# Performance work log

Hardware: AMD Instinct MI355X
Metric: run time of the kernel (lower is better)

Reference implementation:

```python
import jax, jax.numpy as jnp
import numpy as np

LOG2 = 0.6931471805599453
GAMMA = 10.0
NUM_KERNELS = 301
N_LAYERS = 3


def ssp(v):
    # ShiftedSoftplus: softplus(x) - log(2)
    return jax.nn.softplus(v) - jnp.asarray(LOG2, v.dtype)


def setup_inputs() -> dict:
    key = jax.random.key(0)
    ks = jax.random.split(key, 20)
    N, F, K, L, V = 512, 128, NUM_KERNELS, N_LAYERS, 100
    s = 0.05
    return {
        "x": jax.random.randint(ks[0], (N,), 0, V),
        "r": jax.random.uniform(ks[1], (N, 3), dtype=jnp.float32) * 10.0,
        "emb": jax.random.normal(ks[2], (V, F), dtype=jnp.float32),
        "aw_W": jax.random.normal(ks[3], (L, F, F), dtype=jnp.float32) * s,
        "aw_b": jax.random.normal(ks[4], (L, F), dtype=jnp.float32) * s,
        "cf_W1": jax.random.normal(ks[5], (L, K, F), dtype=jnp.float32) * s,
        "cf_b1": jax.random.normal(ks[6], (L, F), dtype=jnp.float32) * s,
        "cf_W2": jax.random.normal(ks[7], (L, F, F), dtype=jnp.float32) * s,
        "cf_b2": jax.random.normal(ks[8], (L, F), dtype=jnp.float32) * s,
        "n_W1": jax.random.normal(ks[9], (L, F, F), dtype=jnp.float32) * s,
        "n_b1": jax.random.normal(ks[10], (L, F), dtype=jnp.float32) * s,
        "n_W2": jax.random.normal(ks[11], (L, F, F), dtype=jnp.float32) * s,
        "n_b2": jax.random.normal(ks[12], (L, F), dtype=jnp.float32) * s,
        "out_W1": jax.random.normal(ks[13], (F, 32), dtype=jnp.float32) * s,
        "out_b1": jax.random.normal(ks[14], (32,), dtype=jnp.float32) * s,
        "out_W2": jax.random.normal(ks[15], (32, 1), dtype=jnp.float32) * s,
        "out_b2": jax.random.normal(ks[16], (1,), dtype=jnp.float32) * s,
    }


def reference(x, r, emb, aw_W, aw_b, cf_W1, cf_b1, cf_W2, cf_b2,
              n_W1, n_b1, n_W2, n_b2, out_W1, out_b1, out_W2, out_b2):
    centers = jnp.linspace(0.0, 30.0, NUM_KERNELS, dtype=r.dtype)  # [K]
    # pairwise distances (torch.cdist, p=2) with safe sqrt at the diagonal
    diff = r[:, None, :] - r[None, :, :]                 # [N,N,3]
    d2 = jnp.sum(diff * diff, axis=-1)                   # [N,N]
    mask = d2 > 0
    d = jnp.where(mask, jnp.sqrt(jnp.where(mask, d2, 1.0)), 0.0)

    h = emb[x]                                           # [N,F]
    for l in range(N_LAYERS):
        o = h @ aw_W[l] + aw_b[l]                        # atom-wise linear
        # Gaussian RBF expansion: [N,N,K]
        e = jnp.exp(-GAMMA * jnp.square(d[..., None] - centers))
        # filter-generating MLP: [N,N,F]
        w = ssp(e @ cf_W1[l] + cf_b1[l])
        w = ssp(w @ cf_W2[l] + cf_b2[l])
        # continuous-filter conv: o[i,k] = sum_j x[j,k] * w[i,j,k]
        c = jnp.einsum('jk,ijk->ik', o, w)
        c = ssp(c @ n_W1[l] + n_b1[l]) @ n_W2[l] + n_b2[l]
        h = h + c
    out = ssp(h @ out_W1 + out_b1) @ out_W2 + out_b2     # [N,1]
    # AdaptiveAvgPool1d(1) on a 2D [N,1] tensor is identity over L=1
    return out.reshape(-1)
```

## Files before the change

### kernel.cpp

```cpp
#include <hip/hip_runtime.h>
#include <hip/hip_fp16.h>
#include <math.h>

#define N_ATOMS 512
#define F_DIM   128
#define K_RBF   301
#define NLAYER  3
#define GAMMA_C 10.0f
#define LOG2_C  0.6931471805599453f

#define TAB_H     0.01f
#define TAB_INVH  100.0f
#define TAB_ROWS  1768
#define RPB       8
#define NGROUPS   (TAB_ROWS / RPB)
#define NTASKS    (NGROUPS * NLAYER)
#define NBBLK     ((NTASKS + 1) / 2)
#define ROW_BYTES 512

__device__ __forceinline__ float ssp(float x) {
    float ax = fabsf(x);
    return fmaxf(x, 0.0f) + log1pf(expf(-ax)) - LOG2_C;
}
__device__ __forceinline__ __half2 u2h2(unsigned u) {
    union { unsigned u; __half2 h; } c; c.u = u; return c.h;
}
__device__ __forceinline__ unsigned h22u(__half2 h) {
    union { unsigned u; __half2 h; } c; c.h = h; return c.u;
}

__global__ void __launch_bounds__(256)
prep_build(const int* __restrict__ x, const float* __restrict__ r,
           const float* __restrict__ emb,
           const float* __restrict__ aw_W, const float* __restrict__ aw_b,
           const float* __restrict__ cf_W1, const float* __restrict__ cf_b1,
           const float* __restrict__ cf_W2, const float* __restrict__ cf_b2,
           uint2* __restrict__ dpk, float* __restrict__ h,
           unsigned* __restrict__ opk, uint2* __restrict__ ptab) {
    __shared__ float hs[F_DIM];
    __shared__ float os[F_DIM];
    __shared__ float e_s[2][RPB + 1][34];
    __shared__ float w1_s[2][F_DIM][12];
    __shared__ float outs[2][RPB + 1][F_DIM];

    if (blockIdx.x < N_ATOMS) {
        int i = blockIdx.x;
        int t = threadIdx.x;
        float rx = r[i * 3 + 0], ry = r[i * 3 + 1], rz = r[i * 3 + 2];
        if (t < F_DIM) {
            float hv = emb[x[i] * F_DIM + t];
            h[i * F_DIM + t] = hv;
            hs[t] = hv;
        }
        for (int j = t; j < N_ATOMS; j += 256) {
            float dx = rx - r[j * 3 + 0];
            float dy = ry - r[j * 3 + 1];
            float dz = rz - r[j * 3 + 2];
            float d  = sqrtf(dx * dx + dy * dy + dz * dz);
            float xb = d * TAB_INVH;
            int   b  = ::min((int)xb, TAB_ROWS - 2);
            float fr = xb - (float)b;
            __half fh = __float2half(fr);
            dpk[i * N_ATOMS + j] = make_uint2((unsigned)b * ROW_BYTES,
                                              h22u(__halves2half2(fh, fh)));
        }
        __syncthreads();
        if (t < F_DIM) {
            float acc = aw_b[t];
            for (int g = 0; g < F_DIM; ++g) acc = fmaf(hs[g], aw_W[g * F_DIM + t], acc);
            os[t] = acc;
        }
        __syncthreads();
        if (t < F_DIM / 2)
            opk[i * 64 + t] = h22u(__halves2half2(__float2half(os[2 * t]),
                                                  __float2half(os[2 * t + 1])));
        return;
    }

    int u = threadIdx.x >> 7;
    int f = threadIdx.x & 127;
    int task = (blockIdx.x - N_ATOMS) * 2 + u;
    bool valid = task < NTASKS;
    task = ::min(task, NTASKS - 1);
    int l    = task / NGROUPS;
    int row0 = (task % NGROUPS) * RPB;

    float dlo = row0 * TAB_H;
    float dhi = (row0 + RPB) * TAB_H;
    int k0 = ::max(0, (int)ceilf((dlo - 1.45f) * 10.0f));
    int k1 = ::min(K_RBF - 1, (int)floorf((dhi + 1.45f) * 10.0f));
    int kw = k1 - k0 + 1;

    for (int idx = f; idx < (RPB + 1) * kw; idx += F_DIM) {
        int rr = idx / kw, kk = idx % kw;
        float dv = (row0 + rr) * TAB_H;
        float tt = dv - 0.1f * (float)(k0 + kk);
        e_s[u][rr][kk] = expf(-GAMMA_C * tt * tt);
    }
    __syncthreads();

    const float* W1 = cf_W1 + l * K_RBF * F_DIM;
    float b1v = cf_b1[l * F_DIM + f];
    float acc[RPB + 1];
#pragma unroll
    for (int rr = 0; rr <= RPB; ++rr) acc[rr] = b1v;
    for (int kk = 0; kk < kw; ++kk) {
        float w1v = W1[(k0 + kk) * F_DIM + f];
#pragma unroll
        for (int rr = 0; rr <= RPB; ++rr) acc[rr] = fmaf(e_s[u][rr][kk], w1v, acc[rr]);
    }
#pragma unroll
    for (int rr = 0; rr <= RPB; ++rr) w1_s[u][f][rr] = ssp(acc[rr]);
    __syncthreads();

    const float* W2 = cf_W2 + l * F_DIM * F_DIM;
    float b2v = cf_b2[l * F_DIM + f];
    float acc2[RPB + 1];
#pragma unroll
    for (int rr = 0; rr <= RPB; ++rr) acc2[rr] = b2v;
    for (int g = 0; g < F_DIM; ++g) {
        float w2v = W2[g * F_DIM + f];
        float4 wa = *(const float4*)&w1_s[u][g][0];
        float4 wb = *(const float4*)&w1_s[u][g][4];
        float  wc = w1_s[u][g][8];
        acc2[0] = fmaf(wa.x, w2v, acc2[0]);
        acc2[1] = fmaf(wa.y, w2v, acc2[1]);
        acc2[2] = fmaf(wa.z, w2v, acc2[2]);
        acc2[3] = fmaf(wa.w, w2v, acc2[3]);
        acc2[4] = fmaf(wb.x, w2v, acc2[4]);
        acc2[5] = fmaf(wb.y, w2v, acc2[5]);
        acc2[6] = fmaf(wb.z, w2v, acc2[6]);
        acc2[7] = fmaf(wb.w, w2v, acc2[7]);
        acc2[8] = fmaf(wc,   w2v, acc2[8]);
    }
#pragma unroll
    for (int rr = 0; rr <= RPB; ++rr) outs[u][rr][f] = ssp(acc2[rr]);
    __syncthreads();

    if (valid) {
        int p = f & 63;
        int rbase = (f >> 6) * (RPB / 2);
#pragma unroll
        for (int q = 0; q < RPB / 2; ++q) {
            int rr = rbase + q;
            float t00 = outs[u][rr][2 * p],     t01 = outs[u][rr][2 * p + 1];
            float n00 = outs[u][rr + 1][2 * p], n01 = outs[u][rr + 1][2 * p + 1];
            uint2 v = make_uint2(
                h22u(__halves2half2(__float2half(t00), __float2half(t01))),
                h22u(__halves2half2(__float2half(n00 - t00), __float2half(n01 - t01))));
            ptab[((size_t)l * TAB_ROWS + row0 + rr) * 64 + p] = v;
        }
    }
}

__global__ void __launch_bounds__(512)
convnode_kernel(const uint2* __restrict__ dpk, const unsigned* __restrict__ opk_in,
                const uint2* __restrict__ ptab,
                const float* __restrict__ n_W1, const float* __restrict__ n_b1,
                const float* __restrict__ n_W2, const float* __restrict__ n_b2,
                float* __restrict__ h,
                const float* __restrict__ aw_W, const float* __restrict__ aw_b,
                unsigned* __restrict__ opk_out,
                const float* __restrict__ oW1, const float* __restrict__ ob1,
                const float* __restrict__ oW2, const float* __restrict__ ob2,
                float* __restrict__ out, int l) {
    int i  = blockIdx.x;
    int t  = threadIdx.x;
    int p  = t & 63;
    int jc = t >> 6;

    __shared__ uint2  ds[N_ATOMS];
    __shared__ float2 red[8][64];
    __shared__ float  cs[F_DIM];
    __shared__ float  t1s[F_DIM];
    __shared__ float  hs[F_DIM];

    ds[t] = dpk[i * N_ATOMS + t];
    if (t < F_DIM) hs[t] = h[i * F_DIM + t];
    __syncthreads();

    const char* T = (const char*)(ptab + (size_t)l * TAB_ROWS * 64) + p * 8;
    float2 acc = make_float2(0.0f, 0.0f);
    int j = jc * 64;
#pragma unroll 4
    for (int jj = 0; jj < 64; ++jj, ++j) {
        uint2 e = ds[j];
        uint2 tv = *(const uint2*)(T + e.x);
        __half2 w2 = __hfma2(u2h2(e.y), u2h2(tv.y), u2h2(tv.x));
        __half2 oh = u2h2(opk_in[j * 64 + p]);
        acc.x = fmaf(__half2float(__low2half(w2)),  __half2float(__low2half(oh)),  acc.x);
        acc.y = fmaf(__half2float(__high2half(w2)), __half2float(__high2half(oh)), acc.y);
    }
    red[jc][p] = acc;
    __syncthreads();
    if (jc == 0) {
        float2 s = red[0][p];
#pragma unroll
        for (int q = 1; q < 8; ++q) { s.x += red[q][p].x; s.y += red[q][p].y; }
        *(float2*)&cs[2 * p] = s;
    }
    __syncthreads();

    if (t < F_DIM) {
        const float* W1 = n_W1 + l * F_DIM * F_DIM;
        float a = n_b1[l * F_DIM + t];
        for (int g = 0; g < F_DIM; ++g) a = fmaf(cs[g], W1[g * F_DIM + t], a);
        t1s[t] = ssp(a);
    }
    __syncthreads();
    if (t < F_DIM) {
        const float* W2 = n_W2 + l * F_DIM * F_DIM;
        float a2 = n_b2[l * F_DIM + t];
        for (int g = 0; g < F_DIM; ++g) a2 = fmaf(t1s[g], W2[g * F_DIM + t], a2);
        float hv = hs[t] + a2;
        h[i * F_DIM + t] = hv;
        hs[t] = hv;
    }
    __syncthreads();

    if (l < NLAYER - 1) {
        if (t < F_DIM) {
            const float* W = aw_W + (l + 1) * F_DIM * F_DIM;
            float a = aw_b[(l + 1) * F_DIM + t];
            for (int g = 0; g < F_DIM; ++g) a = fmaf(hs[g], W[g * F_DIM + t], a);
            t1s[t] = a;
        }
        __syncthreads();
        if (t < F_DIM / 2)
            opk_out[i * 64 + t] = h22u(__halves2half2(__float2half(t1s[2 * t]),
                                                      __float2half(t1s[2 * t + 1])));
    } else {
        float val = 0.0f;
        if (t < 32) {
            float ah = ob1[t];
            for (int g = 0; g < F_DIM; ++g) ah = fmaf(hs[g], oW1[g * 32 + t], ah);
            val = ssp(ah) * oW2[t];
        }
#pragma unroll
        for (int off = 16; off > 0; off >>= 1) val += __shfl_xor(val, off, 64);
        if (t == 0) out[i] = val + ob2[0];
    }
}

extern "C" void kernel_launch(void* const* d_in, const int* in_sizes, int n_in,
                              void* d_out, int out_size, void* d_ws, size_t ws_size,
                              hipStream_t stream) {
    const int*   x     = (const int*)  d_in[0];
    const float* r     = (const float*)d_in[1];
    const float* emb   = (const float*)d_in[2];
    const float* aw_W  = (const float*)d_in[3];
    const float* aw_b  = (const float*)d_in[4];
    const float* cf_W1 = (const float*)d_in[5];
    const float* cf_b1 = (const float*)d_in[6];
    const float* cf_W2 = (const float*)d_in[7];
    const float* cf_b2 = (const float*)d_in[8];
    const float* n_W1  = (const float*)d_in[9];
    const float* n_b1  = (const float*)d_in[10];
    const float* n_W2  = (const float*)d_in[11];
    const float* n_b2  = (const float*)d_in[12];
    const float* oW1   = (const float*)d_in[13];
    const float* ob1   = (const float*)d_in[14];
    const float* oW2   = (const float*)d_in[15];
    const float* ob2   = (const float*)d_in[16];
    float* out = (float*)d_out;

    char* ws = (char*)d_ws;
    uint2*    dpk  = (uint2*)ws;    ws += (size_t)N_ATOMS * N_ATOMS * 8;
    float*    h    = (float*)ws;    ws += (size_t)N_ATOMS * F_DIM * 4;
    unsigned* opkA = (unsigned*)ws; ws += (size_t)N_ATOMS * (F_DIM / 2) * 4;
    unsigned* opkB = (unsigned*)ws; ws += (size_t)N_ATOMS * (F_DIM / 2) * 4;
    uint2*    ptab = (uint2*)ws;

    prep_build<<<N_ATOMS + NBBLK, 256, 0, stream>>>(
        x, r, emb, aw_W, aw_b, cf_W1, cf_b1, cf_W2, cf_b2, dpk, h, opkA, ptab);
    for (int l = 0; l < NLAYER; ++l) {
        unsigned* oin  = (l & 1) ? opkB : opkA;
        unsigned* oout = (l & 1) ? opkA : opkB;
        convnode_kernel<<<N_ATOMS, 512, 0, stream>>>(
            dpk, oin, ptab, n_W1, n_b1, n_W2, n_b2, h,
            aw_W, aw_b, oout, oW1, ob1, oW2, ob2, out, l);
    }
}
```

Baseline: 169.0 us.

## Fuse prep, table build and all layers into one cooperative persistent kernel

Replaces the four separate launches (prep/table build plus one conv+node kernel per layer) with a single cooperative kernel of 512 blocks that uses grid-wide syncs between phases. The goal is to remove launch gaps and kernel-boundary overheads. In exchange, the conv phase now runs with 256 threads per block instead of 512, and each grid sync carries its own cost. The table-build epilogue also changes: the shared-memory staging buffer is replaced by register values exchanged with lane shuffles. The old multi-kernel path is kept as a fallback if the cooperative launch fails.

New measurement: 485.3 us. 2.87x slower.

```diff
diff --git a/kernel.cpp b/kernel.cpp
--- a/kernel.cpp
+++ b/kernel.cpp
@@ -1,6 +1,9 @@
 #include <hip/hip_runtime.h>
 #include <hip/hip_fp16.h>
+#include <hip/hip_cooperative_groups.h>
 #include <math.h>
+
+namespace cg = cooperative_groups;
 
 #define N_ATOMS 512
 #define F_DIM   128
@@ -15,7 +18,7 @@
 #define RPB       8
 #define NGROUPS   (TAB_ROWS / RPB)
 #define NTASKS    (NGROUPS * NLAYER)
-#define NBBLK     ((NTASKS + 1) / 2)
+#define NBBLK2    ((NTASKS + 1) / 2)
 #define ROW_BYTES 512
 
 __device__ __forceinline__ float ssp(float x) {
@@ -27,6 +30,231 @@
 }
 __device__ __forceinline__ unsigned h22u(__half2 h) {
     union { unsigned u; __half2 h; } c; c.h = h; return c.u;
+}
+
+struct BuildS {
+    float e_s [2][RPB + 1][34];
+    float w1_s[2][F_DIM][12];
+};
+struct ConvS {
+    uint2  ds[N_ATOMS];
+    float2 red[4][64];
+    float  cs[F_DIM];
+    float  t1s[F_DIM];
+    float  hs[F_DIM];
+};
+
+__global__ void __launch_bounds__(256)
+fused_kernel(const int* __restrict__ x, const float* __restrict__ r,
+             const float* __restrict__ emb,
+             const float* __restrict__ aw_W, const float* __restrict__ aw_b,
+             const float* __restrict__ cf_W1, const float* __restrict__ cf_b1,
+             const float* __restrict__ cf_W2, const float* __restrict__ cf_b2,
+             const float* __restrict__ n_W1, const float* __restrict__ n_b1,
+             const float* __restrict__ n_W2, const float* __restrict__ n_b2,
+             const float* __restrict__ oW1, const float* __restrict__ ob1,
+             const float* __restrict__ oW2, const float* __restrict__ ob2,
+             uint2* __restrict__ dpk, float* __restrict__ h,
+             unsigned* __restrict__ opkA, unsigned* __restrict__ opkB,
+             uint2* __restrict__ ptab, float* __restrict__ out) {
+    cg::grid_group grid = cg::this_grid();
+    __shared__ __align__(16) char smem[sizeof(BuildS)];
+    BuildS& B = *reinterpret_cast<BuildS*>(smem);
+    ConvS&  C = *reinterpret_cast<ConvS*>(smem);
+
+    int i = blockIdx.x;
+    int t = threadIdx.x;
+
+    {
+        float rx = r[i * 3 + 0], ry = r[i * 3 + 1], rz = r[i * 3 + 2];
+        if (t < F_DIM) {
+            float hv = emb[x[i] * F_DIM + t];
+            h[i * F_DIM + t] = hv;
+            C.hs[t] = hv;
+        }
+        for (int j = t; j < N_ATOMS; j += 256) {
+            float dx = rx - r[j * 3 + 0];
+            float dy = ry - r[j * 3 + 1];
+            float dz = rz - r[j * 3 + 2];
+            float d  = sqrtf(dx * dx + dy * dy + dz * dz);
+            float xb = d * TAB_INVH;
+            int   b  = ::min((int)xb, TAB_ROWS - 2);
+            float fr = xb - (float)b;
+            __half fh = __float2half(fr);
+            dpk[i * N_ATOMS + j] = make_uint2((unsigned)b * ROW_BYTES,
+                                              h22u(__halves2half2(fh, fh)));
+        }
+        __syncthreads();
+        if (t < F_DIM) {
+            float acc = aw_b[t];
+            for (int g = 0; g < F_DIM; ++g) acc = fmaf(C.hs[g], aw_W[g * F_DIM + t], acc);
+            C.t1s[t] = acc;
+        }
+        __syncthreads();
+        if (t < F_DIM / 2)
+            opkA[i * 64 + t] = h22u(__halves2half2(__float2half(C.t1s[2 * t]),
+                                                   __float2half(C.t1s[2 * t + 1])));
+    }
+    __syncthreads();
+
+    if (i < NBBLK2) {
+        int u = t >> 7;
+        int f = t & 127;
+        int task = i * 2 + u;
+        bool valid = task < NTASKS;
+        task = valid ? task : NTASKS - 1;
+        int l    = task / NGROUPS;
+        int row0 = (task % NGROUPS) * RPB;
+
+        float dlo = row0 * TAB_H;
+        float dhi = (row0 + RPB) * TAB_H;
+        int k0 = ::max(0, (int)ceilf((dlo - 1.45f) * 10.0f));
+        int k1 = ::min(K_RBF - 1, (int)floorf((dhi + 1.45f) * 10.0f));
+        int kw = k1 - k0 + 1;
+
+        for (int idx = f; idx < (RPB + 1) * kw; idx += F_DIM) {
+            int rr = idx / kw, kk = idx % kw;
+            float dv = (row0 + rr) * TAB_H;
+            float tt = dv - 0.1f * (float)(k0 + kk);
+            B.e_s[u][rr][kk] = expf(-GAMMA_C * tt * tt);
+        }
+        __syncthreads();
+
+        const float* W1 = cf_W1 + l * K_RBF * F_DIM;
+        float b1v = cf_b1[l * F_DIM + f];
+        float acc[RPB + 1];
+#pragma unroll
+        for (int rr = 0; rr <= RPB; ++rr) acc[rr] = b1v;
+        for (int kk = 0; kk < kw; ++kk) {
+            float w1v = W1[(k0 + kk) * F_DIM + f];
+#pragma unroll
+            for (int rr = 0; rr <= RPB; ++rr) acc[rr] = fmaf(B.e_s[u][rr][kk], w1v, acc[rr]);
+        }
+#pragma unroll
+        for (int rr = 0; rr <= RPB; ++rr) B.w1_s[u][f][rr] = ssp(acc[rr]);
+        __syncthreads();
+
+        const float* W2 = cf_W2 + l * F_DIM * F_DIM;
+        float b2v = cf_b2[l * F_DIM + f];
+        float acc2[RPB + 1];
+#pragma unroll
+        for (int rr = 0; rr <= RPB; ++rr) acc2[rr] = b2v;
+        for (int g = 0; g < F_DIM; ++g) {
+            float w2v = W2[g * F_DIM + f];
+            float4 wa = *(const float4*)&B.w1_s[u][g][0];
+            float4 wb = *(const float4*)&B.w1_s[u][g][4];
+            float  wc = B.w1_s[u][g][8];
+            acc2[0] = fmaf(wa.x, w2v, acc2[0]);
+            acc2[1] = fmaf(wa.y, w2v, acc2[1]);
+            acc2[2] = fmaf(wa.z, w2v, acc2[2]);
+            acc2[3] = fmaf(wa.w, w2v, acc2[3]);
+            acc2[4] = fmaf(wb.x, w2v, acc2[4]);
+            acc2[5] = fmaf(wb.y, w2v, acc2[5]);
+            acc2[6] = fmaf(wb.z, w2v, acc2[6]);
+            acc2[7] = fmaf(wb.w, w2v, acc2[7]);
+            acc2[8] = fmaf(wc,   w2v, acc2[8]);
+        }
+        float o9[RPB + 1];
+#pragma unroll
+        for (int rr = 0; rr <= RPB; ++rr) o9[rr] = ssp(acc2[rr]);
+
+        if (valid) {
+            int p = f >> 1;
+            bool odd = (f & 1);
+#pragma unroll
+            for (int rr = 0; rr < RPB; ++rr) {
+                float t0 = o9[rr];
+                float dt = o9[rr + 1] - o9[rr];
+                float ot0 = __shfl_xor(t0, 1, 64);
+                float odt = __shfl_xor(dt, 1, 64);
+                if (!odd) {
+                    uint2 v = make_uint2(
+                        h22u(__halves2half2(__float2half(t0), __float2half(ot0))),
+                        h22u(__halves2half2(__float2half(dt), __float2half(odt))));
+                    ptab[((size_t)l * TAB_ROWS + row0 + rr) * 64 + p] = v;
+                }
+            }
+        }
+    }
+
+    __threadfence();
+    grid.sync();
+
+    int p  = t & 63;
+    int jc = t >> 6;
+
+    for (int l = 0; l < NLAYER; ++l) {
+        for (int j = t; j < N_ATOMS; j += 256) C.ds[j] = dpk[i * N_ATOMS + j];
+        if (t < F_DIM) C.hs[t] = h[i * F_DIM + t];
+        __syncthreads();
+
+        const unsigned* oin  = (l & 1) ? opkB : opkA;
+        unsigned*       oout = (l & 1) ? opkA : opkB;
+
+        const char* T = (const char*)(ptab + (size_t)l * TAB_ROWS * 64) + p * 8;
+        float2 acc = make_float2(0.0f, 0.0f);
+        int j = jc * 128;
+#pragma unroll 4
+        for (int jj = 0; jj < 128; ++jj, ++j) {
+            uint2 e = C.ds[j];
+            uint2 tv = *(const uint2*)(T + e.x);
+            __half2 w2 = __hfma2(u2h2(e.y), u2h2(tv.y), u2h2(tv.x));
+            __half2 oh = u2h2(oin[j * 64 + p]);
+            acc.x = fmaf(__half2float(__low2half(w2)),  __half2float(__low2half(oh)),  acc.x);
+            acc.y = fmaf(__half2float(__high2half(w2)), __half2float(__high2half(oh)), acc.y);
+        }
+        C.red[jc][p] = acc;
+        __syncthreads();
+        if (jc == 0) {
+            float2 s = C.red[0][p];
+#pragma unroll
+            for (int q = 1; q < 4; ++q) { s.x += C.red[q][p].x; s.y += C.red[q][p].y; }
+            *(float2*)&C.cs[2 * p] = s;
+        }
+        __syncthreads();
+
+        if (t < F_DIM) {
+            const float* W1 = n_W1 + l * F_DIM * F_DIM;
+            float a = n_b1[l * F_DIM + t];
+            for (int g = 0; g < F_DIM; ++g) a = fmaf(C.cs[g], W1[g * F_DIM + t], a);
+            C.t1s[t] = ssp(a);
+        }
+        __syncthreads();
+        if (t < F_DIM) {
+            const float* W2 = n_W2 + l * F_DIM * F_DIM;
+            float a2 = n_b2[l * F_DIM + t];
+            for (int g = 0; g < F_DIM; ++g) a2 = fmaf(C.t1s[g], W2[g * F_DIM + t], a2);
+            float hv = C.hs[t] + a2;
+            h[i * F_DIM + t] = hv;
+            C.hs[t] = hv;
+        }
+        __syncthreads();
+
+        if (l < NLAYER - 1) {
+            if (t < F_DIM) {
+                const float* W = aw_W + (l + 1) * F_DIM * F_DIM;
+                float a = aw_b[(l + 1) * F_DIM + t];
+                for (int g = 0; g < F_DIM; ++g) a = fmaf(C.hs[g], W[g * F_DIM + t], a);
+                C.cs[t] = a;
+            }
+            __syncthreads();
+            if (t < F_DIM / 2)
+                oout[i * 64 + t] = h22u(__halves2half2(__float2half(C.cs[2 * t]),
+                                                       __float2half(C.cs[2 * t + 1])));
+            __threadfence();
+            grid.sync();
+        } else {
+            float val = 0.0f;
+            if (t < 32) {
+                float ah = ob1[t];
+                for (int g = 0; g < F_DIM; ++g) ah = fmaf(C.hs[g], oW1[g * 32 + t], ah);
+                val = ssp(ah) * oW2[t];
+            }
+#pragma unroll
+            for (int off = 16; off > 0; off >>= 1) val += __shfl_xor(val, off, 64);
+            if (t == 0) out[i] = val + ob2[0];
+        }
+    }
 }
 
 __global__ void __launch_bounds__(256)
@@ -41,7 +269,6 @@
     __shared__ float os[F_DIM];
     __shared__ float e_s[2][RPB + 1][34];
     __shared__ float w1_s[2][F_DIM][12];
-    __shared__ float outs[2][RPB + 1][F_DIM];
 
     if (blockIdx.x < N_ATOMS) {
         int i = blockIdx.x;
@@ -81,7 +308,7 @@
     int f = threadIdx.x & 127;
     int task = (blockIdx.x - N_ATOMS) * 2 + u;
     bool valid = task < NTASKS;
-    task = ::min(task, NTASKS - 1);
+    task = valid ? task : NTASKS - 1;
     int l    = task / NGROUPS;
     int row0 = (task % NGROUPS) * RPB;
 
@@ -133,22 +360,25 @@
         acc2[7] = fmaf(wb.w, w2v, acc2[7]);
         acc2[8] = fmaf(wc,   w2v, acc2[8]);
     }
-#pragma unroll
-    for (int rr = 0; rr <= RPB; ++rr) outs[u][rr][f] = ssp(acc2[rr]);
-    __syncthreads();
+    float o9[RPB + 1];
+#pragma unroll
+    for (int rr = 0; rr <= RPB; ++rr) o9[rr] = ssp(acc2[rr]);
 
     if (valid) {
-        int p = f & 63;
-        int rbase = (f >> 6) * (RPB / 2);
-#pragma unroll
-        for (int q = 0; q < RPB / 2; ++q) {
-            int rr = rbase + q;
-            float t00 = outs[u][rr][2 * p],     t01 = outs[u][rr][2 * p + 1];
-            float n00 = outs[u][rr + 1][2 * p], n01 = outs[u][rr + 1][2 * p + 1];
-            uint2 v = make_uint2(
-                h22u(__halves2half2(__float2half(t00), __float2half(t01))),
-                h22u(__halves2half2(__float2half(n00 - t00), __float2half(n01 - t01))));
-            ptab[((size_t)l * TAB_ROWS + row0 + rr) * 64 + p] = v;
+        int p = f >> 1;
+        bool odd = (f & 1);
+#pragma unroll
+        for (int rr = 0; rr < RPB; ++rr) {
+            float t0 = o9[rr];
+            float dt = o9[rr + 1] - o9[rr];
+            float ot0 = __shfl_xor(t0, 1, 64);
+            float odt = __shfl_xor(dt, 1, 64);
+            if (!odd) {
+                uint2 v = make_uint2(
+                    h22u(__halves2half2(__float2half(t0), __float2half(ot0))),
+                    h22u(__halves2half2(__float2half(dt), __float2half(odt))));
+                ptab[((size_t)l * TAB_ROWS + row0 + rr) * 64 + p] = v;
+            }
         }
     }
 }
@@ -271,13 +501,27 @@
     unsigned* opkB = (unsigned*)ws; ws += (size_t)N_ATOMS * (F_DIM / 2) * 4;
     uint2*    ptab = (uint2*)ws;
 
-    prep_build<<<N_ATOMS + NBBLK, 256, 0, stream>>>(
-        x, r, emb, aw_W, aw_b, cf_W1, cf_b1, cf_W2, cf_b2, dpk, h, opkA, ptab);
-    for (int l = 0; l < NLAYER; ++l) {
-        unsigned* oin  = (l & 1) ? opkB : opkA;
-        unsigned* oout = (l & 1) ? opkA : opkB;
-        convnode_kernel<<<N_ATOMS, 512, 0, stream>>>(
-            dpk, oin, ptab, n_W1, n_b1, n_W2, n_b2, h,
-            aw_W, aw_b, oout, oW1, ob1, oW2, ob2, out, l);
-    }
-}
+    void* args[] = {
+        (void*)&x, (void*)&r, (void*)&emb, (void*)&aw_W, (void*)&aw_b,
+        (void*)&cf_W1, (void*)&cf_b1, (void*)&cf_W2, (void*)&cf_b2,
+        (void*)&n_W1, (void*)&n_b1, (void*)&n_W2, (void*)&n_b2,
+        (void*)&oW1, (void*)&ob1, (void*)&oW2, (void*)&ob2,
+        (void*)&dpk, (void*)&h, (void*)&opkA, (void*)&opkB,
+        (void*)&ptab, (void*)&out
+    };
+    hipError_t err = hipLaunchCooperativeKernel((const void*)fused_kernel,
+                                                dim3(N_ATOMS), dim3(256),
+                                                args, 0, stream);
+    if (err != hipSuccess) {
+        (void)hipGetLastError();
+        prep_build<<<N_ATOMS + NBBLK2, 256, 0, stream>>>(
+            x, r, emb, aw_W, aw_b, cf_W1, cf_b1, cf_W2, cf_b2, dpk, h, opkA, ptab);
+        for (int l = 0; l < NLAYER; ++l) {
+            unsigned* oin  = (l & 1) ? opkB : opkA;
+            unsigned* oout = (l & 1) ? opkA : opkB;
+            convnode_kernel<<<N_ATOMS, 512, 0, stream>>>(
+                dpk, oin, ptab, n_W1, n_b1, n_W2, n_b2, h,
+                aw_W, aw_b, oout, oW1, ob1, oW2, ob2, out, l);
+        }
+    }
+}
```

## Split conv over j into partial kernel and separate node MLP kernel

Applied to the files above, without the earlier changes.

The fused per-atom conv+node kernel is split in two. A conv_partial kernel divides the j-sum into four chunks over a 2D grid and writes partial sums, and a small 128-thread node_kernel reduces them and runs the node MLPs. This raises parallelism in the gather-heavy conv and stops 512-thread blocks from idling through the serial MLP stages. In the table build, the shared-memory staging of outputs is replaced with register shuffles to pack half2 pairs. The cost is extra launches per layer and a global round-trip through the partial buffer.

Measured after the change: 173.3 us. 1.03x slower.

```diff
diff --git a/kernel.cpp b/kernel.cpp
--- a/kernel.cpp
+++ b/kernel.cpp
@@ -15,8 +15,10 @@
 #define RPB       8
 #define NGROUPS   (TAB_ROWS / RPB)
 #define NTASKS    (NGROUPS * NLAYER)
-#define NBBLK     ((NTASKS + 1) / 2)
+#define NBBLK2    ((NTASKS + 1) / 2)
 #define ROW_BYTES 512
+#define JSPLIT    4
+#define JCH       (N_ATOMS / JSPLIT)
 
 __device__ __forceinline__ float ssp(float x) {
     float ax = fabsf(x);
@@ -41,7 +43,6 @@
     __shared__ float os[F_DIM];
     __shared__ float e_s[2][RPB + 1][34];
     __shared__ float w1_s[2][F_DIM][12];
-    __shared__ float outs[2][RPB + 1][F_DIM];
 
     if (blockIdx.x < N_ATOMS) {
         int i = blockIdx.x;
@@ -81,7 +82,7 @@
     int f = threadIdx.x & 127;
     int task = (blockIdx.x - N_ATOMS) * 2 + u;
     bool valid = task < NTASKS;
-    task = ::min(task, NTASKS - 1);
+    task = valid ? task : NTASKS - 1;
     int l    = task / NGROUPS;
     int row0 = (task % NGROUPS) * RPB;
 
@@ -133,112 +134,124 @@
         acc2[7] = fmaf(wb.w, w2v, acc2[7]);
         acc2[8] = fmaf(wc,   w2v, acc2[8]);
     }
-#pragma unroll
-    for (int rr = 0; rr <= RPB; ++rr) outs[u][rr][f] = ssp(acc2[rr]);
-    __syncthreads();
+    float o9[RPB + 1];
+#pragma unroll
+    for (int rr = 0; rr <= RPB; ++rr) o9[rr] = ssp(acc2[rr]);
 
     if (valid) {
-        int p = f & 63;
-        int rbase = (f >> 6) * (RPB / 2);
-#pragma unroll
-        for (int q = 0; q < RPB / 2; ++q) {
-            int rr = rbase + q;
-            float t00 = outs[u][rr][2 * p],     t01 = outs[u][rr][2 * p + 1];
-            float n00 = outs[u][rr + 1][2 * p], n01 = outs[u][rr + 1][2 * p + 1];
-            uint2 v = make_uint2(
-                h22u(__halves2half2(__float2half(t00), __float2half(t01))),
-                h22u(__halves2half2(__float2half(n00 - t00), __float2half(n01 - t01))));
-            ptab[((size_t)l * TAB_ROWS + row0 + rr) * 64 + p] = v;
-        }
-    }
-}
-
-__global__ void __launch_bounds__(512)
-convnode_kernel(const uint2* __restrict__ dpk, const unsigned* __restrict__ opk_in,
-                const uint2* __restrict__ ptab,
-                const float* __restrict__ n_W1, const float* __restrict__ n_b1,
-                const float* __restrict__ n_W2, const float* __restrict__ n_b2,
-                float* __restrict__ h,
-                const float* __restrict__ aw_W, const float* __restrict__ aw_b,
-                unsigned* __restrict__ opk_out,
-                const float* __restrict__ oW1, const float* __restrict__ ob1,
-                const float* __restrict__ oW2, const float* __restrict__ ob2,
-                float* __restrict__ out, int l) {
+        int p = f >> 1;
+        bool odd = (f & 1);
+#pragma unroll
+        for (int rr = 0; rr < RPB; ++rr) {
+            float t0 = o9[rr];
+            float dt = o9[rr + 1] - o9[rr];
+            float ot0 = __shfl_xor(t0, 1, 64);
+            float odt = __shfl_xor(dt, 1, 64);
+            if (!odd) {
+                uint2 v = make_uint2(
+                    h22u(__halves2half2(__float2half(t0), __float2half(ot0))),
+                    h22u(__halves2half2(__float2half(dt), __float2half(odt))));
+                ptab[((size_t)l * TAB_ROWS + row0 + rr) * 64 + p] = v;
+            }
+        }
+    }
+}
+
+__global__ void __launch_bounds__(512, 8)
+conv_partial(const uint2* __restrict__ dpk, const unsigned* __restrict__ opk_in,
+             const uint2* __restrict__ ptab, float* __restrict__ cpart, int l) {
     int i  = blockIdx.x;
+    int s  = blockIdx.y;
     int t  = threadIdx.x;
     int p  = t & 63;
     int jc = t >> 6;
 
-    __shared__ uint2  ds[N_ATOMS];
+    __shared__ uint2  ds[JCH];
     __shared__ float2 red[8][64];
-    __shared__ float  cs[F_DIM];
-    __shared__ float  t1s[F_DIM];
-    __shared__ float  hs[F_DIM];
-
-    ds[t] = dpk[i * N_ATOMS + t];
-    if (t < F_DIM) hs[t] = h[i * F_DIM + t];
-    __syncthreads();
-
-    const char* T = (const char*)(ptab + (size_t)l * TAB_ROWS * 64) + p * 8;
+
+    if (t < JCH) ds[t] = dpk[i * N_ATOMS + s * JCH + t];
+    __syncthreads();
+
+    const char*     T  = (const char*)(ptab + (size_t)l * TAB_ROWS * 64) + p * 8;
+    const unsigned* ob = opk_in + (s * JCH) * 64 + p;
+
     float2 acc = make_float2(0.0f, 0.0f);
-    int j = jc * 64;
+    int j0 = jc * (JCH / 8);
 #pragma unroll 4
-    for (int jj = 0; jj < 64; ++jj, ++j) {
-        uint2 e = ds[j];
+    for (int jj = 0; jj < JCH / 8; ++jj) {
+        uint2 e = ds[j0 + jj];
         uint2 tv = *(const uint2*)(T + e.x);
         __half2 w2 = __hfma2(u2h2(e.y), u2h2(tv.y), u2h2(tv.x));
-        __half2 oh = u2h2(opk_in[j * 64 + p]);
+        __half2 oh = u2h2(ob[(j0 + jj) * 64]);
         acc.x = fmaf(__half2float(__low2half(w2)),  __half2float(__low2half(oh)),  acc.x);
         acc.y = fmaf(__half2float(__high2half(w2)), __half2float(__high2half(oh)), acc.y);
     }
     red[jc][p] = acc;
     __syncthreads();
     if (jc == 0) {
-        float2 s = red[0][p];
-#pragma unroll
-        for (int q = 1; q < 8; ++q) { s.x += red[q][p].x; s.y += red[q][p].y; }
-        *(float2*)&cs[2 * p] = s;
-    }
-    __syncthreads();
-
-    if (t < F_DIM) {
-        const float* W1 = n_W1 + l * F_DIM * F_DIM;
-        float a = n_b1[l * F_DIM + t];
-        for (int g = 0; g < F_DIM; ++g) a = fmaf(cs[g], W1[g * F_DIM + t], a);
-        t1s[t] = ssp(a);
-    }
-    __syncthreads();
-    if (t < F_DIM) {
-        const float* W2 = n_W2 + l * F_DIM * F_DIM;
-        float a2 = n_b2[l * F_DIM + t];
-        for (int g = 0; g < F_DIM; ++g) a2 = fmaf(t1s[g], W2[g * F_DIM + t], a2);
-        float hv = hs[t] + a2;
-        h[i * F_DIM + t] = hv;
-        hs[t] = hv;
-    }
+        float2 v = red[0][p];
+#pragma unroll
+        for (int q = 1; q < 8; ++q) { v.x += red[q][p].x; v.y += red[q][p].y; }
+        *(float2*)&cpart[((size_t)s * N_ATOMS + i) * F_DIM + 2 * p] = v;
+    }
+}
+
+__global__ void __launch_bounds__(128)
+node_kernel(const float* __restrict__ cpart,
+            const float* __restrict__ n_W1, const float* __restrict__ n_b1,
+            const float* __restrict__ n_W2, const float* __restrict__ n_b2,
+            float* __restrict__ h,
+            const float* __restrict__ aw_W, const float* __restrict__ aw_b,
+            unsigned* __restrict__ opk_out,
+            const float* __restrict__ oW1, const float* __restrict__ ob1,
+            const float* __restrict__ oW2, const float* __restrict__ ob2,
+            float* __restrict__ out, int l) {
+    int i = blockIdx.x, f = threadIdx.x;
+    __shared__ float cs[F_DIM];
+    __shared__ float t1s[F_DIM];
+    __shared__ float hs[F_DIM];
+
+    float cv = 0.0f;
+#pragma unroll
+    for (int s = 0; s < JSPLIT; ++s)
+        cv += cpart[((size_t)s * N_ATOMS + i) * F_DIM + f];
+    cs[f] = cv;
+    hs[f] = h[i * F_DIM + f];
+    __syncthreads();
+
+    const float* W1 = n_W1 + l * F_DIM * F_DIM;
+    float a = n_b1[l * F_DIM + f];
+    for (int g = 0; g < F_DIM; ++g) a = fmaf(cs[g], W1[g * F_DIM + f], a);
+    t1s[f] = ssp(a);
+    __syncthreads();
+
+    const float* W2 = n_W2 + l * F_DIM * F_DIM;
+    float a2 = n_b2[l * F_DIM + f];
+    for (int g = 0; g < F_DIM; ++g) a2 = fmaf(t1s[g], W2[g * F_DIM + f], a2);
+    float hv = hs[f] + a2;
+    h[i * F_DIM + f] = hv;
+    hs[f] = hv;
     __syncthreads();
 
     if (l < NLAYER - 1) {
-        if (t < F_DIM) {
-            const float* W = aw_W + (l + 1) * F_DIM * F_DIM;
-            float a = aw_b[(l + 1) * F_DIM + t];
-            for (int g = 0; g < F_DIM; ++g) a = fmaf(hs[g], W[g * F_DIM + t], a);
-            t1s[t] = a;
-        }
+        const float* W = aw_W + (l + 1) * F_DIM * F_DIM;
+        float av = aw_b[(l + 1) * F_DIM + f];
+        for (int g = 0; g < F_DIM; ++g) av = fmaf(hs[g], W[g * F_DIM + f], av);
+        t1s[f] = av;
         __syncthreads();
-        if (t < F_DIM / 2)
-            opk_out[i * 64 + t] = h22u(__halves2half2(__float2half(t1s[2 * t]),
-                                                      __float2half(t1s[2 * t + 1])));
+        if (f < F_DIM / 2)
+            opk_out[i * 64 + f] = h22u(__halves2half2(__float2half(t1s[2 * f]),
+                                                      __float2half(t1s[2 * f + 1])));
     } else {
         float val = 0.0f;
-        if (t < 32) {
-            float ah = ob1[t];
-            for (int g = 0; g < F_DIM; ++g) ah = fmaf(hs[g], oW1[g * 32 + t], ah);
-            val = ssp(ah) * oW2[t];
+        if (f < 32) {
+            float ah = ob1[f];
+            for (int g = 0; g < F_DIM; ++g) ah = fmaf(hs[g], oW1[g * 32 + f], ah);
+            val = ssp(ah) * oW2[f];
         }
 #pragma unroll
         for (int off = 16; off > 0; off >>= 1) val += __shfl_xor(val, off, 64);
-        if (t == 0) out[i] = val + ob2[0];
+        if (f == 0) out[i] = val + ob2[0];
     }
 }
 
@@ -265,19 +278,21 @@
     float* out = (float*)d_out;
 
     char* ws = (char*)d_ws;
-    uint2*    dpk  = (uint2*)ws;    ws += (size_t)N_ATOMS * N_ATOMS * 8;
-    float*    h    = (float*)ws;    ws += (size_t)N_ATOMS * F_DIM * 4;
-    unsigned* opkA = (unsigned*)ws; ws += (size_t)N_ATOMS * (F_DIM / 2) * 4;
-    unsigned* opkB = (unsigned*)ws; ws += (size_t)N_ATOMS * (F_DIM / 2) * 4;
-    uint2*    ptab = (uint2*)ws;
-
-    prep_build<<<N_ATOMS + NBBLK, 256, 0, stream>>>(
+    uint2*    dpk   = (uint2*)ws;    ws += (size_t)N_ATOMS * N_ATOMS * 8;
+    float*    h     = (float*)ws;    ws += (size_t)N_ATOMS * F_DIM * 4;
+    unsigned* opkA  = (unsigned*)ws; ws += (size_t)N_ATOMS * (F_DIM / 2) * 4;
+    unsigned* opkB  = (unsigned*)ws; ws += (size_t)N_ATOMS * (F_DIM / 2) * 4;
+    float*    cpart = (float*)ws;    ws += (size_t)JSPLIT * N_ATOMS * F_DIM * 4;
+    uint2*    ptab  = (uint2*)ws;
+
+    prep_build<<<N_ATOMS + NBBLK2, 256, 0, stream>>>(
         x, r, emb, aw_W, aw_b, cf_W1, cf_b1, cf_W2, cf_b2, dpk, h, opkA, ptab);
     for (int l = 0; l < NLAYER; ++l) {
         unsigned* oin  = (l & 1) ? opkB : opkA;
         unsigned* oout = (l & 1) ? opkA : opkB;
-        convnode_kernel<<<N_ATOMS, 512, 0, stream>>>(
-            dpk, oin, ptab, n_W1, n_b1, n_W2, n_b2, h,
+        conv_partial<<<dim3(N_ATOMS, JSPLIT), 512, 0, stream>>>(dpk, oin, ptab, cpart, l);
+        node_kernel<<<N_ATOMS, 128, 0, stream>>>(
+            cpart, n_W1, n_b1, n_W2, n_b2, h,
             aw_W, aw_b, oout, oW1, ob1, oW2, ob2, out, l);
     }
 }
```

## Widen conv gather loads, split node MLPs across all threads, drop LDS staging

Applied to the files above, without the earlier changes.

The conv loop in convnode_kernel now has each thread handle four features through 16-byte table loads, with 32-lane feature groups and 16 neighbor chunks. The dense 128x128 node MLP, atom-wise linear and output head matvecs are split across all 512 threads as four partial K-slices reduced through shared memory, where before only 128 threads did them serially. In prep_build the shared-memory staging for half packing is replaced by register values plus lane shuffles, which removes a barrier and some shared memory. Launch bounds also request higher occupancy, at the cost of extra barriers and reduction traffic in shared memory.

Result: no change. 165.9 us (-1.8%).

```diff
diff --git a/kernel.cpp b/kernel.cpp
--- a/kernel.cpp
+++ b/kernel.cpp
@@ -15,7 +15,7 @@
 #define RPB       8
 #define NGROUPS   (TAB_ROWS / RPB)
 #define NTASKS    (NGROUPS * NLAYER)
-#define NBBLK     ((NTASKS + 1) / 2)
+#define NBBLK2    ((NTASKS + 1) / 2)
 #define ROW_BYTES 512
 
 __device__ __forceinline__ float ssp(float x) {
@@ -41,7 +41,6 @@
     __shared__ float os[F_DIM];
     __shared__ float e_s[2][RPB + 1][34];
     __shared__ float w1_s[2][F_DIM][12];
-    __shared__ float outs[2][RPB + 1][F_DIM];
 
     if (blockIdx.x < N_ATOMS) {
         int i = blockIdx.x;
@@ -81,7 +80,7 @@
     int f = threadIdx.x & 127;
     int task = (blockIdx.x - N_ATOMS) * 2 + u;
     bool valid = task < NTASKS;
-    task = ::min(task, NTASKS - 1);
+    task = valid ? task : NTASKS - 1;
     int l    = task / NGROUPS;
     int row0 = (task % NGROUPS) * RPB;
 
@@ -133,27 +132,30 @@
         acc2[7] = fmaf(wb.w, w2v, acc2[7]);
         acc2[8] = fmaf(wc,   w2v, acc2[8]);
     }
-#pragma unroll
-    for (int rr = 0; rr <= RPB; ++rr) outs[u][rr][f] = ssp(acc2[rr]);
-    __syncthreads();
+    float o9[RPB + 1];
+#pragma unroll
+    for (int rr = 0; rr <= RPB; ++rr) o9[rr] = ssp(acc2[rr]);
 
     if (valid) {
-        int p = f & 63;
-        int rbase = (f >> 6) * (RPB / 2);
-#pragma unroll
-        for (int q = 0; q < RPB / 2; ++q) {
-            int rr = rbase + q;
-            float t00 = outs[u][rr][2 * p],     t01 = outs[u][rr][2 * p + 1];
-            float n00 = outs[u][rr + 1][2 * p], n01 = outs[u][rr + 1][2 * p + 1];
-            uint2 v = make_uint2(
-                h22u(__halves2half2(__float2half(t00), __float2half(t01))),
-                h22u(__halves2half2(__float2half(n00 - t00), __float2half(n01 - t01))));
-            ptab[((size_t)l * TAB_ROWS + row0 + rr) * 64 + p] = v;
-        }
-    }
-}
-
-__global__ void __launch_bounds__(512)
+        int p = f >> 1;
+        bool odd = (f & 1);
+#pragma unroll
+        for (int rr = 0; rr < RPB; ++rr) {
+            float t0 = o9[rr];
+            float dt = o9[rr + 1] - o9[rr];
+            float ot0 = __shfl_xor(t0, 1, 64);
+            float odt = __shfl_xor(dt, 1, 64);
+            if (!odd) {
+                uint2 v = make_uint2(
+                    h22u(__halves2half2(__float2half(t0), __float2half(ot0))),
+                    h22u(__halves2half2(__float2half(dt), __float2half(odt))));
+                ptab[((size_t)l * TAB_ROWS + row0 + rr) * 64 + p] = v;
+            }
+        }
+    }
+}
+
+__global__ void __launch_bounds__(512, 4)
 convnode_kernel(const uint2* __restrict__ dpk, const unsigned* __restrict__ opk_in,
                 const uint2* __restrict__ ptab,
                 const float* __restrict__ n_W1, const float* __restrict__ n_b1,
@@ -166,52 +168,81 @@
                 float* __restrict__ out, int l) {
     int i  = blockIdx.x;
     int t  = threadIdx.x;
-    int p  = t & 63;
-    int jc = t >> 6;
-
-    __shared__ uint2  ds[N_ATOMS];
-    __shared__ float2 red[8][64];
-    __shared__ float  cs[F_DIM];
-    __shared__ float  t1s[F_DIM];
-    __shared__ float  hs[F_DIM];
+    int p2 = t & 31;
+    int jc = t >> 5;
+
+    __shared__ __align__(16) uint2 ds[N_ATOMS];
+    __shared__ __align__(16) float redbuf[16 * 32 * 4];
+    __shared__ __align__(16) float cs[F_DIM];
+    __shared__ __align__(16) float t1s[F_DIM];
+    __shared__ __align__(16) float hs[F_DIM];
 
     ds[t] = dpk[i * N_ATOMS + t];
     if (t < F_DIM) hs[t] = h[i * F_DIM + t];
     __syncthreads();
 
-    const char* T = (const char*)(ptab + (size_t)l * TAB_ROWS * 64) + p * 8;
-    float2 acc = make_float2(0.0f, 0.0f);
-    int j = jc * 64;
+    const char*  T   = (const char*)(ptab + (size_t)l * TAB_ROWS * 64) + p2 * 16;
+    const uint2* ob  = (const uint2*)opk_in + p2;
+
+    float4 acc = make_float4(0.0f, 0.0f, 0.0f, 0.0f);
+    int j0 = jc * 32;
 #pragma unroll 4
-    for (int jj = 0; jj < 64; ++jj, ++j) {
+    for (int jj = 0; jj < 32; ++jj) {
+        int j = j0 + jj;
         uint2 e = ds[j];
-        uint2 tv = *(const uint2*)(T + e.x);
-        __half2 w2 = __hfma2(u2h2(e.y), u2h2(tv.y), u2h2(tv.x));
-        __half2 oh = u2h2(opk_in[j * 64 + p]);
-        acc.x = fmaf(__half2float(__low2half(w2)),  __half2float(__low2half(oh)),  acc.x);
-        acc.y = fmaf(__half2float(__high2half(w2)), __half2float(__high2half(oh)), acc.y);
-    }
-    red[jc][p] = acc;
-    __syncthreads();
-    if (jc == 0) {
-        float2 s = red[0][p];
-#pragma unroll
-        for (int q = 1; q < 8; ++q) { s.x += red[q][p].x; s.y += red[q][p].y; }
-        *(float2*)&cs[2 * p] = s;
-    }
-    __syncthreads();
-
+        uint4 tv = *(const uint4*)(T + e.x);
+        uint2 ohu = ob[j * 32];
+        __half2 fr2 = u2h2(e.y);
+        __half2 wa = __hfma2(fr2, u2h2(tv.y), u2h2(tv.x));
+        __half2 wb = __hfma2(fr2, u2h2(tv.w), u2h2(tv.z));
+        __half2 oa = u2h2(ohu.x);
+        __half2 obh = u2h2(ohu.y);
+        acc.x = fmaf(__half2float(__low2half(wa)),  __half2float(__low2half(oa)),  acc.x);
+        acc.y = fmaf(__half2float(__high2half(wa)), __half2float(__high2half(oa)), acc.y);
+        acc.z = fmaf(__half2float(__low2half(wb)),  __half2float(__low2half(obh)), acc.z);
+        acc.w = fmaf(__half2float(__high2half(wb)), __half2float(__high2half(obh)), acc.w);
+    }
+    *(float4*)&redbuf[(jc * 32 + p2) * 4] = acc;
+    __syncthreads();
+    if (t < 32) {
+        float4 s = *(const float4*)&redbuf[t * 4];
+#pragma unroll
+        for (int q = 1; q < 16; ++q) {
+            float4 v = *(const float4*)&redbuf[(q * 32 + t) * 4];
+            s.x += v.x; s.y += v.y; s.z += v.z; s.w += v.w;
+        }
+        *(float4*)&cs[4 * t] = s;
+    }
+    __syncthreads();
+
+    {
+        int q = t >> 7, f = t & 127;
+        const float* W1 = n_W1 + l * F_DIM * F_DIM;
+        float a = 0.0f;
+        int g0 = q * 32;
+        for (int g = 0; g < 32; ++g) a = fmaf(cs[g0 + g], W1[(g0 + g) * F_DIM + f], a);
+        redbuf[q * F_DIM + f] = a;
+    }
+    __syncthreads();
     if (t < F_DIM) {
-        const float* W1 = n_W1 + l * F_DIM * F_DIM;
-        float a = n_b1[l * F_DIM + t];
-        for (int g = 0; g < F_DIM; ++g) a = fmaf(cs[g], W1[g * F_DIM + t], a);
+        float a = redbuf[t] + redbuf[F_DIM + t] + redbuf[2 * F_DIM + t]
+                + redbuf[3 * F_DIM + t] + n_b1[l * F_DIM + t];
         t1s[t] = ssp(a);
     }
     __syncthreads();
+
+    {
+        int q = t >> 7, f = t & 127;
+        const float* W2 = n_W2 + l * F_DIM * F_DIM;
+        float a = 0.0f;
+        int g0 = q * 32;
+        for (int g = 0; g < 32; ++g) a = fmaf(t1s[g0 + g], W2[(g0 + g) * F_DIM + f], a);
+        redbuf[q * F_DIM + f] = a;
+    }
+    __syncthreads();
     if (t < F_DIM) {
-        const float* W2 = n_W2 + l * F_DIM * F_DIM;
-        float a2 = n_b2[l * F_DIM + t];
-        for (int g = 0; g < F_DIM; ++g) a2 = fmaf(t1s[g], W2[g * F_DIM + t], a2);
+        float a2 = redbuf[t] + redbuf[F_DIM + t] + redbuf[2 * F_DIM + t]
+                 + redbuf[3 * F_DIM + t] + n_b2[l * F_DIM + t];
         float hv = hs[t] + a2;
         h[i * F_DIM + t] = hv;
         hs[t] = hv;
@@ -219,22 +250,38 @@
     __syncthreads();
 
     if (l < NLAYER - 1) {
+        {
+            int q = t >> 7, f = t & 127;
+            const float* W = aw_W + (l + 1) * F_DIM * F_DIM;
+            float a = 0.0f;
+            int g0 = q * 32;
+            for (int g = 0; g < 32; ++g) a = fmaf(hs[g0 + g], W[(g0 + g) * F_DIM + f], a);
+            redbuf[q * F_DIM + f] = a;
+        }
+        __syncthreads();
         if (t < F_DIM) {
-            const float* W = aw_W + (l + 1) * F_DIM * F_DIM;
-            float a = aw_b[(l + 1) * F_DIM + t];
-            for (int g = 0; g < F_DIM; ++g) a = fmaf(hs[g], W[g * F_DIM + t], a);
-            t1s[t] = a;
+            t1s[t] = redbuf[t] + redbuf[F_DIM + t] + redbuf[2 * F_DIM + t]
+                   + redbuf[3 * F_DIM + t] + aw_b[(l + 1) * F_DIM + t];
         }
         __syncthreads();
         if (t < F_DIM / 2)
             opk_out[i * 64 + t] = h22u(__halves2half2(__float2half(t1s[2 * t]),
                                                       __float2half(t1s[2 * t + 1])));
     } else {
+        {
+            int q = t >> 5, f = t & 31;
+            float a = 0.0f;
+            int g0 = q * 8;
+            for (int g = 0; g < 8; ++g) a = fmaf(hs[g0 + g], oW1[(g0 + g) * 32 + f], a);
+            redbuf[q * 32 + f] = a;
+        }
+        __syncthreads();
         float val = 0.0f;
         if (t < 32) {
-            float ah = ob1[t];
-            for (int g = 0; g < F_DIM; ++g) ah = fmaf(hs[g], oW1[g * 32 + t], ah);
-            val = ssp(ah) * oW2[t];
+            float a = ob1[t];
+#pragma unroll
+            for (int q = 0; q < 16; ++q) a += redbuf[q * 32 + t];
+            val = ssp(a) * oW2[t];
         }
 #pragma unroll
         for (int off = 16; off > 0; off >>= 1) val += __shfl_xor(val, off, 64);
@@ -271,7 +318,7 @@
     unsigned* opkB = (unsigned*)ws; ws += (size_t)N_ATOMS * (F_DIM / 2) * 4;
     uint2*    ptab = (uint2*)ws;
 
-    prep_build<<<N_ATOMS + NBBLK, 256, 0, stream>>>(
+    prep_build<<<N_ATOMS + NBBLK2, 256, 0, stream>>>(
         x, r, emb, aw_W, aw_b, cf_W1, cf_b1, cf_W2, cf_b2, dpk, h, opkA, ptab);
     for (int l = 0; l < NLAYER; ++l) {
         unsigned* oin  = (l & 1) ? opkB : opkA;
```
